# Optimization experiments

Hardware: AMD Instinct MI355X
Metric: run time of the kernel (lower is better)

## Reference

```python
import jax, jax.numpy as jnp
import numpy as np

N_NODES = 100000
N_EDGES = 3200000
D_FEAT = 256
N_CLASS = 40


def setup_inputs() -> dict:
    key = jax.random.key(0)
    ks = jax.random.split(key, 12)
    x = jax.random.normal(ks[0], (N_NODES, D_FEAT), dtype=jnp.float32)
    edge_src = jax.random.randint(ks[1], (N_EDGES,), 0, N_NODES, dtype=jnp.int32)
    edge_dst = jax.random.randint(ks[2], (N_EDGES,), 0, N_NODES, dtype=jnp.int32)
    edge_weight = jax.random.uniform(ks[3], (N_EDGES,), dtype=jnp.float32)
    s = 1.0 / np.sqrt(D_FEAT)
    W1 = jax.random.normal(ks[4], (D_FEAT, D_FEAT), dtype=jnp.float32) * s
    b1 = jax.random.normal(ks[5], (D_FEAT,), dtype=jnp.float32) * s
    W2 = jax.random.normal(ks[6], (D_FEAT, D_FEAT), dtype=jnp.float32) * s
    b2 = jax.random.normal(ks[7], (D_FEAT,), dtype=jnp.float32) * s
    W3 = jax.random.normal(ks[8], (D_FEAT, D_FEAT), dtype=jnp.float32) * s
    b3 = jax.random.normal(ks[9], (D_FEAT,), dtype=jnp.float32) * s
    Wd = jax.random.normal(ks[10], (D_FEAT, N_CLASS), dtype=jnp.float32) * s
    bd = jax.random.normal(ks[11], (N_CLASS,), dtype=jnp.float32) * s
    return {"x": x, "edge_src": edge_src, "edge_dst": edge_dst,
            "edge_weight": edge_weight, "W1": W1, "b1": b1, "W2": W2,
            "b2": b2, "W3": W3, "b3": b3, "Wd": Wd, "bd": bd}


def reference(x, edge_src, edge_dst, edge_weight, W1, b1, W2, b2, W3, b3, Wd, bd):
    n = x.shape[0]

    def spmm(h):  # sparse adj @ h  via gather + segment-sum on dst
        return jax.ops.segment_sum(edge_weight[:, None] * h[edge_src], edge_dst,
                                   num_segments=n)

    # GraphConvolution: adj @ (x @ W) + b, then ReLU (dropout is eval-mode identity)
    h = jax.nn.relu(spmm(x @ W1) + b1)
    h = jax.nn.relu(spmm(h @ W2) + b2)
    h = jax.nn.relu(spmm(h @ W3) + b3)
    return h @ Wd + bd
```

## Files before the change

### kernel.cpp

```cpp
#include <hip/hip_runtime.h>

#define D 256
#define NCLS 40
#define CAP 96
#define KB 391
#define CAPB 9216

typedef __attribute__((ext_vector_type(8))) short bf16x8;
typedef __attribute__((ext_vector_type(4))) float f32x4;

__device__ __forceinline__ unsigned short f2b(float f) {
    unsigned u = __float_as_uint(f);
    u += 0x7fffu + ((u >> 16) & 1u);
    return (unsigned short)(u >> 16);
}
__device__ __forceinline__ float b2f(unsigned short s) {
    return __uint_as_float(((unsigned)s) << 16);
}

__global__ __launch_bounds__(256) void bin_pass1(const int* __restrict__ src,
                                                 const int* __restrict__ dst,
                                                 const float* __restrict__ w, int ne,
                                                 int* __restrict__ bcur,
                                                 int2* __restrict__ binned) {
    __shared__ int cnt[KB], base[KB], cnt2[KB];
    const int tid = threadIdx.x;
    const int e0 = blockIdx.x * 8192;
    for (int i = tid; i < KB; i += 256) { cnt[i] = 0; cnt2[i] = 0; }
    __syncthreads();
    for (int i = tid; i < 8192; i += 256) {
        int e = e0 + i;
        if (e < ne) atomicAdd(&cnt[dst[e] >> 8], 1);
    }
    __syncthreads();
    for (int i = tid; i < KB; i += 256) {
        int c = cnt[i];
        base[i] = c ? atomicAdd(&bcur[i], c) : 0;
    }
    __syncthreads();
    for (int i = tid; i < 8192; i += 256) {
        int e = e0 + i;
        if (e < ne) {
            int d = dst[e];
            int b = d >> 8;
            int slot = base[b] + atomicAdd(&cnt2[b], 1);
            if (slot < CAPB)
                binned[(size_t)b * CAPB + slot] =
                    make_int2((src[e] & 0x1ffff) | ((d & 255) << 17), __float_as_int(w[e]));
        }
    }
}

__global__ __launch_bounds__(256) void bin_pass2(const int2* __restrict__ binned,
                                                 const int* __restrict__ bcur,
                                                 int* __restrict__ cursor,
                                                 int2* __restrict__ pairs, int M) {
    __shared__ int cur[256];
    const int b = blockIdx.x;
    const int tid = threadIdx.x;
    cur[tid] = 0;
    __syncthreads();
    int n = bcur[b]; if (n > CAPB) n = CAPB;
    const int2* rec = binned + (size_t)b * CAPB;
    const int dbase = b << 8;
    for (int i = tid; i < n; i += 256) {
        int2 rc = rec[i];
        int dl = (rc.x >> 17) & 255;
        int s = rc.x & 0x1ffff;
        int r = atomicAdd(&cur[dl], 1);
        if (r < CAP) pairs[(size_t)(dbase + dl) * CAP + r] = make_int2(s, rc.y);
    }
    __syncthreads();
    int d = dbase + tid;
    if (d < M) cursor[d] = min(cur[tid], CAP);
}

__global__ __launch_bounds__(256) void prep_weights3x(const float* __restrict__ W1,
                                                      const float* __restrict__ W2,
                                                      const float* __restrict__ W3,
                                                      short* __restrict__ B1,
                                                      short* __restrict__ B2,
                                                      short* __restrict__ B3) {
    int gi = blockIdx.x * 256 + threadIdx.x;
    int which = gi >> 16;
    int i = gi & 65535;
    const float* W = (which == 0) ? W1 : (which == 1) ? W2 : W3;
    short* Bp      = (which == 0) ? B1 : (which == 1) ? B2 : B3;
    int e = i & 7, lane = (i >> 3) & 63, t = (i >> 9) & 15, ks = (i >> 13) & 7;
    int n = t * 16 + (lane & 15);
    int k = ks * 32 + ((lane >> 4) & 3) * 8 + e;
    Bp[i] = (short)f2b(W[k * D + n]);
}

__global__ __launch_bounds__(256) void prep_wd(const float* __restrict__ Wd,
                                               short* __restrict__ Wdp) {
    int i = blockIdx.x * 256 + threadIdx.x;
    int e = i & 7, lane = (i >> 3) & 63;
    int q = i >> 9;
    int t = q % 3, hl = (q / 3) & 1, ks = q / 6;
    int n = t * 16 + (lane & 15);
    int k = ks * 32 + ((lane >> 4) & 3) * 8 + e;
    float v = (n < NCLS) ? Wd[k * NCLS + n] : 0.f;
    unsigned short hi = f2b(v);
    Wdp[i] = hl ? (short)f2b(v - b2f(hi)) : (short)hi;
}

template<int AFP32>
__global__ __launch_bounds__(256) void gemm_mfma6(const float* __restrict__ A32,
                                                  const short* __restrict__ A16,
                                                  const short* __restrict__ Bpack,
                                                  short* __restrict__ Cout, int M,
                                                  float* __restrict__ sAbs) {
    __shared__ short Bs[2][16384];
    const int tid = threadIdx.x;
    const int lane = tid & 63;
    const int r = lane & 15, kg = lane >> 4;
    const int wv = tid >> 6;
    const int row_base = blockIdx.x * 128 + wv * 32;
    int ar0 = row_base + r;      if (ar0 >= M) ar0 = M - 1;
    int ar1 = row_base + 16 + r; if (ar1 >= M) ar1 = M - 1;

    f32x4 acc0[16], acc1[16];
#pragma unroll
    for (int t = 0; t < 16; t++) {
        acc0[t] = (f32x4){0.f, 0.f, 0.f, 0.f};
        acc1[t] = (f32x4){0.f, 0.f, 0.f, 0.f};
    }

    bf16x8 af0[8], af1[8];
    if (!AFP32) {
#pragma unroll
        for (int ks = 0; ks < 8; ks++) {
            af0[ks] = *(const bf16x8*)(A16 + (size_t)ar0 * D + ks * 32 + kg * 8);
            af1[ks] = *(const bf16x8*)(A16 + (size_t)ar1 * D + ks * 32 + kg * 8);
        }
    }

    auto stage = [&](int step, int buf) {
        const short* src = Bpack + step * 16384 + tid * 8;
        short* dst = &Bs[buf][tid * 8];
#pragma unroll
        for (int j = 0; j < 8; j++) {
            __builtin_amdgcn_global_load_lds(
                (const __attribute__((address_space(1))) unsigned*)(src + j * 2048),
                (__attribute__((address_space(3))) unsigned*)(dst + j * 2048),
                16, 0, 0);
        }
    };

    stage(0, 0);
#pragma unroll
    for (int step = 0; step < 4; step++) {
        __syncthreads();
        if (step < 3) stage(step + 1, (step + 1) & 1);
#pragma unroll
        for (int kh = 0; kh < 2; kh++) {
            const int ks = step * 2 + kh;
            bf16x8 a0k, a1k;
            if (AFP32) {
                const float* p0 = A32 + (size_t)ar0 * D + ks * 32 + kg * 8;
                const float* p1 = A32 + (size_t)ar1 * D + ks * 32 + kg * 8;
                float4 x0 = *(const float4*)p0, x1 = *(const float4*)(p0 + 4);
                float4 y0 = *(const float4*)p1, y1 = *(const float4*)(p1 + 4);
                a0k[0] = (short)f2b(x0.x); a0k[1] = (short)f2b(x0.y);
                a0k[2] = (short)f2b(x0.z); a0k[3] = (short)f2b(x0.w);
                a0k[4] = (short)f2b(x1.x); a0k[5] = (short)f2b(x1.y);
                a0k[6] = (short)f2b(x1.z); a0k[7] = (short)f2b(x1.w);
                a1k[0] = (short)f2b(y0.x); a1k[1] = (short)f2b(y0.y);
                a1k[2] = (short)f2b(y0.z); a1k[3] = (short)f2b(y0.w);
                a1k[4] = (short)f2b(y1.x); a1k[5] = (short)f2b(y1.y);
                a1k[6] = (short)f2b(y1.z); a1k[7] = (short)f2b(y1.w);
            } else {
                a0k = af0[ks];
                a1k = af1[ks];
            }
#pragma unroll
            for (int t = 0; t < 16; t++) {
                bf16x8 h8 = *(const bf16x8*)&Bs[step & 1][kh * 8192 + t * 512 + lane * 8];
                acc0[t] = __builtin_amdgcn_mfma_f32_16x16x32_bf16(a0k, h8, acc0[t], 0, 0, 0);
                acc1[t] = __builtin_amdgcn_mfma_f32_16x16x32_bf16(a1k, h8, acc1[t], 0, 0, 0);
            }
        }
    }

    float m = 0.f;
#pragma unroll
    for (int t = 0; t < 16; t++) {
#pragma unroll
        for (int rg = 0; rg < 4; rg++) {
            m = fmaxf(m, fabsf(acc0[t][rg]));
            m = fmaxf(m, fabsf(acc1[t][rg]));
        }
    }
#pragma unroll
    for (int off = 32; off >= 1; off >>= 1) m = fmaxf(m, __shfl_xor(m, off));
    if (lane == 0) atomicMax((unsigned int*)sAbs, __float_as_uint(m));

#pragma unroll
    for (int t = 0; t < 16; t++) {
#pragma unroll
        for (int rg = 0; rg < 4; rg++) {
            int o0 = row_base + kg * 4 + rg;
            int o1 = o0 + 16;
            if (o0 < M) Cout[(size_t)o0 * D + t * 16 + r] = (short)f2b(acc0[t][rg]);
            if (o1 < M) Cout[(size_t)o1 * D + t * 16 + r] = (short)f2b(acc1[t][rg]);
        }
    }
}

__global__ __launch_bounds__(256) void quant8(const short* __restrict__ hA,
                                              const float* __restrict__ sAbs,
                                              char* __restrict__ h8, int n) {
    int i = (blockIdx.x * 256 + threadIdx.x) * 16;
    if (i >= n) return;
    const float qs = 127.0f / sAbs[0];
    bf16x8 a = *(const bf16x8*)(hA + i);
    bf16x8 b = *(const bf16x8*)(hA + i + 8);
    unsigned pk[4];
#pragma unroll
    for (int d = 0; d < 4; d++) {
        unsigned v = 0;
#pragma unroll
        for (int j = 0; j < 4; j++) {
            int idx = d * 4 + j;
            float f = b2f((unsigned short)(idx < 8 ? a[idx] : b[idx - 8]));
            int q = __float2int_rn(f * qs);
            q = max(-127, min(127, q));
            v |= ((unsigned)(q & 0xff)) << (j * 8);
        }
        pk[d] = v;
    }
    *(uint4*)(h8 + i) = make_uint4(pk[0], pk[1], pk[2], pk[3]);
}

__global__ __launch_bounds__(256) void spmm8q(const char* __restrict__ h8,
                                              const float* __restrict__ sAbs,
                                              const int* __restrict__ cursor,
                                              const int2* __restrict__ pairs,
                                              const float* __restrict__ bias,
                                              short* __restrict__ out, int M) {
    const int node = blockIdx.x * 16 + (threadIdx.x >> 4);
    if (node >= M) return;
    const int t = threadIdx.x & 15;
    int cnt = cursor[node]; if (cnt > CAP) cnt = CAP;
    const int2* pp = pairs + (size_t)node * CAP;
    const size_t doff = (size_t)t * 16;
    const float sc = sAbs[0] * (1.0f / 127.0f);

    float a[16];
#pragma unroll
    for (int j = 0; j < 16; j++) a[j] = 0.f;

#define ACCD(U, B)                                                         \
    {                                                                      \
        unsigned u = (U);                                                  \
        a[(B) + 0] = fmaf(ws, (float)(int)(char)(u), a[(B) + 0]);          \
        a[(B) + 1] = fmaf(ws, (float)(int)(char)(u >> 8), a[(B) + 1]);     \
        a[(B) + 2] = fmaf(ws, (float)(int)(char)(u >> 16), a[(B) + 2]);    \
        a[(B) + 3] = fmaf(ws, (float)((int)u >> 24), a[(B) + 3]);          \
    }
#define ACCQ(V, WB)                                                        \
    {                                                                      \
        float ws = __int_as_float(WB) * sc;                                \
        ACCD((V).x, 0) ACCD((V).y, 4) ACCD((V).z, 8) ACCD((V).w, 12)       \
    }

    int e = 0;
    for (; e + 8 <= cnt; e += 8) {
        int4 q0 = *(const int4*)(pp + e);
        int4 q1 = *(const int4*)(pp + e + 2);
        int4 q2 = *(const int4*)(pp + e + 4);
        int4 q3 = *(const int4*)(pp + e + 6);
        uint4 v0 = *(const uint4*)(h8 + ((size_t)q0.x << 8) + doff);
        uint4 v1 = *(const uint4*)(h8 + ((size_t)q0.z << 8) + doff);
        uint4 v2 = *(const uint4*)(h8 + ((size_t)q1.x << 8) + doff);
        uint4 v3 = *(const uint4*)(h8 + ((size_t)q1.z << 8) + doff);
        uint4 v4 = *(const uint4*)(h8 + ((size_t)q2.x << 8) + doff);
        uint4 v5 = *(const uint4*)(h8 + ((size_t)q2.z << 8) + doff);
        uint4 v6 = *(const uint4*)(h8 + ((size_t)q3.x << 8) + doff);
        uint4 v7 = *(const uint4*)(h8 + ((size_t)q3.z << 8) + doff);
        ACCQ(v0, q0.y) ACCQ(v1, q0.w) ACCQ(v2, q1.y) ACCQ(v3, q1.w)
        ACCQ(v4, q2.y) ACCQ(v5, q2.w) ACCQ(v6, q3.y) ACCQ(v7, q3.w)
    }
    for (; e < cnt; e++) {
        int2 p = pp[e];
        uint4 v = *(const uint4*)(h8 + ((size_t)p.x << 8) + doff);
        ACCQ(v, p.y)
    }
#undef ACCQ
#undef ACCD

    unsigned o[8];
#pragma unroll
    for (int j = 0; j < 8; j++) {
        float2 b = *(const float2*)(bias + t * 16 + j * 2);
        float r0 = fmaxf(a[j * 2] + b.x, 0.f);
        float r1 = fmaxf(a[j * 2 + 1] + b.y, 0.f);
        o[j] = (unsigned)f2b(r0) | ((unsigned)f2b(r1) << 16);
    }
    uint4* dst = (uint4*)(out + ((size_t)node << 8) + doff);
    dst[0] = make_uint4(o[0], o[1], o[2], o[3]);
    dst[1] = make_uint4(o[4], o[5], o[6], o[7]);
}

__global__ __launch_bounds__(256) void dense_mfma(const short* __restrict__ h,
                                                  const short* __restrict__ Wdp,
                                                  const float* __restrict__ bd,
                                                  float* __restrict__ out, int M) {
    __shared__ short Ws[24576];
    const int tid = threadIdx.x;
    const int lane = tid & 63;
    const int r = lane & 15, kg = lane >> 4;
    const int row_base = blockIdx.x * 64 + (tid >> 6) * 16;
    int arow = row_base + r; if (arow >= M) arow = M - 1;

#pragma unroll
    for (int j = 0; j < 12; j++) {
        __builtin_amdgcn_global_load_lds(
            (const __attribute__((address_space(1))) unsigned*)(Wdp + j * 2048 + tid * 8),
            (__attribute__((address_space(3))) unsigned*)(&Ws[j * 2048 + tid * 8]),
            16, 0, 0);
    }

    f32x4 acc[3];
#pragma unroll
    for (int t = 0; t < 3; t++) acc[t] = (f32x4){0.f, 0.f, 0.f, 0.f};

    bf16x8 af[8];
#pragma unroll
    for (int ks = 0; ks < 8; ks++)
        af[ks] = *(const bf16x8*)(h + (size_t)arow * D + ks * 32 + kg * 8);

    __syncthreads();

#pragma unroll
    for (int ks = 0; ks < 8; ks++) {
#pragma unroll
        for (int t = 0; t < 3; t++) {
            bf16x8 h8 = *(const bf16x8*)&Ws[(ks * 6 + t) * 512 + lane * 8];
            bf16x8 l8 = *(const bf16x8*)&Ws[(ks * 6 + 3 + t) * 512 + lane * 8];
            acc[t] = __builtin_amdgcn_mfma_f32_16x16x32_bf16(af[ks], h8, acc[t], 0, 0, 0);
            acc[t] = __builtin_amdgcn_mfma_f32_16x16x32_bf16(af[ks], l8, acc[t], 0, 0, 0);
        }
    }

#pragma unroll
    for (int t = 0; t < 3; t++) {
#pragma unroll
        for (int rg = 0; rg < 4; rg++) {
            int orow = row_base + kg * 4 + rg;
            int col = t * 16 + r;
            if (orow < M && col < NCLS)
                out[(size_t)orow * NCLS + col] = acc[t][rg] + bd[col];
        }
    }
}


extern "C" void kernel_launch(void* const* d_in, const int* in_sizes, int n_in,
                              void* d_out, int out_size, void* d_ws, size_t ws_size,
                              hipStream_t stream) {
    const float* x    = (const float*)d_in[0];
    const int*   esrc = (const int*)d_in[1];
    const int*   edst = (const int*)d_in[2];
    const float* ew   = (const float*)d_in[3];
    const float* W1   = (const float*)d_in[4];
    const float* b1   = (const float*)d_in[5];
    const float* W2   = (const float*)d_in[6];
    const float* b2   = (const float*)d_in[7];
    const float* W3   = (const float*)d_in[8];
    const float* b3   = (const float*)d_in[9];
    const float* Wd   = (const float*)d_in[10];
    const float* bd   = (const float*)d_in[11];
    float* out = (float*)d_out;

    const int M  = in_sizes[0] / D;
    const int NE = in_sizes[1];

    char* p = (char*)d_ws;
    auto alloc = [&](size_t bytes) -> char* {
        char* r = p;
        p += (bytes + 255) & ~(size_t)255;
        return r;
    };
    short* hA     = (short*)alloc((size_t)M * D * sizeof(short));
    short* hB     = (short*)alloc((size_t)M * D * sizeof(short));
    char*  hA8    = (char*)alloc((size_t)M * D);
    int2*  pairs  = (int2*)alloc((size_t)M * CAP * sizeof(int2));
    int2*  binned = (int2*)alloc((size_t)KB * CAPB * sizeof(int2));
    int*   cursor = (int*)alloc((size_t)M * sizeof(int));
    int*   bcur   = (int*)alloc(KB * sizeof(int));
    float* sAbs   = (float*)alloc(256);
    short* B1p = (short*)alloc(D * D * sizeof(short));
    short* B2p = (short*)alloc(D * D * sizeof(short));
    short* B3p = (short*)alloc(D * D * sizeof(short));
    short* Wdp = (short*)alloc(24576 * sizeof(short));

    hipMemsetAsync(bcur, 0, KB * sizeof(int), stream);
    hipMemsetAsync(sAbs, 0, 256, stream);

    bin_pass1<<<(NE + 8191) / 8192, 256, 0, stream>>>(esrc, edst, ew, NE, bcur, binned);
    bin_pass2<<<KB, 256, 0, stream>>>(binned, bcur, cursor, pairs, M);

    prep_weights3x<<<768, 256, 0, stream>>>(W1, W2, W3, B1p, B2p, B3p);
    prep_wd<<<96, 256, 0, stream>>>(Wd, Wdp);

    const int gg = (M + 127) / 128;
    const int gq = (M * D / 16 + 255) / 256;
    const int gs = (M + 15) / 16;

    gemm_mfma6<1><<<gg, 256, 0, stream>>>(x, nullptr, B1p, hA, M, sAbs + 0);
    quant8<<<gq, 256, 0, stream>>>(hA, sAbs + 0, hA8, M * D);
    spmm8q<<<gs, 256, 0, stream>>>(hA8, sAbs + 0, cursor, pairs, b1, hB, M);

    gemm_mfma6<0><<<gg, 256, 0, stream>>>(nullptr, hB, B2p, hA, M, sAbs + 1);
    quant8<<<gq, 256, 0, stream>>>(hA, sAbs + 1, hA8, M * D);
    spmm8q<<<gs, 256, 0, stream>>>(hA8, sAbs + 1, cursor, pairs, b2, hB, M);

    gemm_mfma6<0><<<gg, 256, 0, stream>>>(nullptr, hB, B3p, hA, M, sAbs + 2);
    quant8<<<gq, 256, 0, stream>>>(hA, sAbs + 2, hA8, M * D);
    spmm8q<<<gs, 256, 0, stream>>>(hA8, sAbs + 2, cursor, pairs, b3, hB, M);

    dense_mfma<<<(M + 63) / 64, 256, 0, stream>>>(hB, Wdp, bd, out, M);
}
```

Measured before the change: 716.7 us.

## Fuse int8 quantization into GEMM epilogue with per-block scales

```diff
diff --git a/kernel.cpp b/kernel.cpp
--- a/kernel.cpp
+++ b/kernel.cpp
@@ -106,12 +106,13 @@
 }
 
 template<int AFP32>
-__global__ __launch_bounds__(256) void gemm_mfma6(const float* __restrict__ A32,
+__global__ __launch_bounds__(256) void gemm_mfma7(const float* __restrict__ A32,
                                                   const short* __restrict__ A16,
                                                   const short* __restrict__ Bpack,
-                                                  short* __restrict__ Cout, int M,
-                                                  float* __restrict__ sAbs) {
+                                                  char* __restrict__ C8, int M,
+                                                  float* __restrict__ scales) {
     __shared__ short Bs[2][16384];
+    __shared__ float red[4];
     const int tid = threadIdx.x;
     const int lane = tid & 63;
     const int r = lane & 15, kg = lane >> 4;
@@ -140,7 +141,14 @@
         const short* src = Bpack + step * 16384 + tid * 8;
         short* dst = &Bs[buf][tid * 8];
 #pragma unroll
-        for (int j = 0; j < 8; j++) {
+        for (int j = 0; j < 4; j++) {
+            __builtin_amdgcn_global_load_lds(
+                (const __attribute__((address_space(1))) unsigned*)(src + j * 2048),
+                (__attribute__((address_space(3))) unsigned*)(dst + j * 2048),
+                16, 0, 0);
+        }
+#pragma unroll
+        for (int j = 4; j < 8; j++) {
             __builtin_amdgcn_global_load_lds(
                 (const __attribute__((address_space(1))) unsigned*)(src + j * 2048),
                 (__attribute__((address_space(3))) unsigned*)(dst + j * 2048),
@@ -194,58 +202,51 @@
     }
 #pragma unroll
     for (int off = 32; off >= 1; off >>= 1) m = fmaxf(m, __shfl_xor(m, off));
-    if (lane == 0) atomicMax((unsigned int*)sAbs, __float_as_uint(m));
-
+    if (lane == 0) red[wv] = m;
+    __syncthreads();
+    float bm = fmaxf(fmaxf(red[0], red[1]), fmaxf(red[2], red[3]));
+    float qs = (bm > 0.f) ? 127.0f / bm : 0.f;
+    if (tid == 0) scales[blockIdx.x] = (bm > 0.f) ? bm * (1.0f / 127.0f) : 1.0f;
+
+    char* Q = (char*)&Bs[0][0];
 #pragma unroll
     for (int t = 0; t < 16; t++) {
 #pragma unroll
         for (int rg = 0; rg < 4; rg++) {
-            int o0 = row_base + kg * 4 + rg;
-            int o1 = o0 + 16;
-            if (o0 < M) Cout[(size_t)o0 * D + t * 16 + r] = (short)f2b(acc0[t][rg]);
-            if (o1 < M) Cout[(size_t)o1 * D + t * 16 + r] = (short)f2b(acc1[t][rg]);
-        }
-    }
-}
-
-__global__ __launch_bounds__(256) void quant8(const short* __restrict__ hA,
-                                              const float* __restrict__ sAbs,
-                                              char* __restrict__ h8, int n) {
-    int i = (blockIdx.x * 256 + threadIdx.x) * 16;
-    if (i >= n) return;
-    const float qs = 127.0f / sAbs[0];
-    bf16x8 a = *(const bf16x8*)(hA + i);
-    bf16x8 b = *(const bf16x8*)(hA + i + 8);
-    unsigned pk[4];
-#pragma unroll
-    for (int d = 0; d < 4; d++) {
-        unsigned v = 0;
-#pragma unroll
-        for (int j = 0; j < 4; j++) {
-            int idx = d * 4 + j;
-            float f = b2f((unsigned short)(idx < 8 ? a[idx] : b[idx - 8]));
-            int q = __float2int_rn(f * qs);
-            q = max(-127, min(127, q));
-            v |= ((unsigned)(q & 0xff)) << (j * 8);
-        }
-        pk[d] = v;
-    }
-    *(uint4*)(h8 + i) = make_uint4(pk[0], pk[1], pk[2], pk[3]);
-}
-
-__global__ __launch_bounds__(256) void spmm8q(const char* __restrict__ h8,
-                                              const float* __restrict__ sAbs,
-                                              const int* __restrict__ cursor,
-                                              const int2* __restrict__ pairs,
-                                              const float* __restrict__ bias,
-                                              short* __restrict__ out, int M) {
+            int rl = wv * 32 + kg * 4 + rg;
+            int q0 = __float2int_rn(acc0[t][rg] * qs);
+            q0 = max(-127, min(127, q0));
+            Q[rl * 272 + t * 16 + r] = (char)q0;
+            int q1 = __float2int_rn(acc1[t][rg] * qs);
+            q1 = max(-127, min(127, q1));
+            Q[(rl + 16) * 272 + t * 16 + r] = (char)q1;
+        }
+    }
+    __syncthreads();
+
+    const int nl = tid >> 1;
+    const int c0 = (tid & 1) * 128;
+    const int grow = blockIdx.x * 128 + nl;
+    if (grow < M) {
+        uint4* dst = (uint4*)(C8 + (size_t)grow * 256 + c0);
+        const char* qs_ = &Q[nl * 272 + c0];
+#pragma unroll
+        for (int j = 0; j < 8; j++) dst[j] = *(const uint4*)(qs_ + j * 16);
+    }
+}
+
+__global__ __launch_bounds__(256) void spmm8q2(const char* __restrict__ h8,
+                                               const float* __restrict__ scales,
+                                               const int* __restrict__ cursor,
+                                               const int2* __restrict__ pairs,
+                                               const float* __restrict__ bias,
+                                               short* __restrict__ out, int M) {
     const int node = blockIdx.x * 16 + (threadIdx.x >> 4);
     if (node >= M) return;
     const int t = threadIdx.x & 15;
     int cnt = cursor[node]; if (cnt > CAP) cnt = CAP;
     const int2* pp = pairs + (size_t)node * CAP;
     const size_t doff = (size_t)t * 16;
-    const float sc = sAbs[0] * (1.0f / 127.0f);
 
     float a[16];
 #pragma unroll
@@ -259,9 +260,9 @@
         a[(B) + 2] = fmaf(ws, (float)(int)(char)(u >> 16), a[(B) + 2]);    \
         a[(B) + 3] = fmaf(ws, (float)((int)u >> 24), a[(B) + 3]);          \
     }
-#define ACCQ(V, WB)                                                        \
+#define ACCQ(V, WB, SRC)                                                   \
     {                                                                      \
-        float ws = __int_as_float(WB) * sc;                                \
+        float ws = __int_as_float(WB) * scales[(SRC) >> 7];                \
         ACCD((V).x, 0) ACCD((V).y, 4) ACCD((V).z, 8) ACCD((V).w, 12)       \
     }
 
@@ -279,13 +280,15 @@
         uint4 v5 = *(const uint4*)(h8 + ((size_t)q2.z << 8) + doff);
         uint4 v6 = *(const uint4*)(h8 + ((size_t)q3.x << 8) + doff);
         uint4 v7 = *(const uint4*)(h8 + ((size_t)q3.z << 8) + doff);
-        ACCQ(v0, q0.y) ACCQ(v1, q0.w) ACCQ(v2, q1.y) ACCQ(v3, q1.w)
-        ACCQ(v4, q2.y) ACCQ(v5, q2.w) ACCQ(v6, q3.y) ACCQ(v7, q3.w)
+        ACCQ(v0, q0.y, q0.x) ACCQ(v1, q0.w, q0.z)
+        ACCQ(v2, q1.y, q1.x) ACCQ(v3, q1.w, q1.z)
+        ACCQ(v4, q2.y, q2.x) ACCQ(v5, q2.w, q2.z)
+        ACCQ(v6, q3.y, q3.x) ACCQ(v7, q3.w, q3.z)
     }
     for (; e < cnt; e++) {
         int2 p = pp[e];
         uint4 v = *(const uint4*)(h8 + ((size_t)p.x << 8) + doff);
-        ACCQ(v, p.y)
+        ACCQ(v, p.y, p.x)
     }
 #undef ACCQ
 #undef ACCD
@@ -383,21 +386,19 @@
         p += (bytes + 255) & ~(size_t)255;
         return r;
     };
-    short* hA     = (short*)alloc((size_t)M * D * sizeof(short));
     short* hB     = (short*)alloc((size_t)M * D * sizeof(short));
     char*  hA8    = (char*)alloc((size_t)M * D);
     int2*  pairs  = (int2*)alloc((size_t)M * CAP * sizeof(int2));
     int2*  binned = (int2*)alloc((size_t)KB * CAPB * sizeof(int2));
     int*   cursor = (int*)alloc((size_t)M * sizeof(int));
     int*   bcur   = (int*)alloc(KB * sizeof(int));
-    float* sAbs   = (float*)alloc(256);
+    float* scales = (float*)alloc(1024 * sizeof(float));
     short* B1p = (short*)alloc(D * D * sizeof(short));
     short* B2p = (short*)alloc(D * D * sizeof(short));
     short* B3p = (short*)alloc(D * D * sizeof(short));
     short* Wdp = (short*)alloc(24576 * sizeof(short));
 
     hipMemsetAsync(bcur, 0, KB * sizeof(int), stream);
-    hipMemsetAsync(sAbs, 0, 256, stream);
 
     bin_pass1<<<(NE + 8191) / 8192, 256, 0, stream>>>(esrc, edst, ew, NE, bcur, binned);
     bin_pass2<<<KB, 256, 0, stream>>>(binned, bcur, cursor, pairs, M);
@@ -406,20 +407,16 @@
     prep_wd<<<96, 256, 0, stream>>>(Wd, Wdp);
 
     const int gg = (M + 127) / 128;
-    const int gq = (M * D / 16 + 255) / 256;
     const int gs = (M + 15) / 16;
 
-    gemm_mfma6<1><<<gg, 256, 0, stream>>>(x, nullptr, B1p, hA, M, sAbs + 0);
-    quant8<<<gq, 256, 0, stream>>>(hA, sAbs + 0, hA8, M * D);
-    spmm8q<<<gs, 256, 0, stream>>>(hA8, sAbs + 0, cursor, pairs, b1, hB, M);
-
-    gemm_mfma6<0><<<gg, 256, 0, stream>>>(nullptr, hB, B2p, hA, M, sAbs + 1);
-    quant8<<<gq, 256, 0, stream>>>(hA, sAbs + 1, hA8, M * D);
-    spmm8q<<<gs, 256, 0, stream>>>(hA8, sAbs + 1, cursor, pairs, b2, hB, M);
-
-    gemm_mfma6<0><<<gg, 256, 0, stream>>>(nullptr, hB, B3p, hA, M, sAbs + 2);
-    quant8<<<gq, 256, 0, stream>>>(hA, sAbs + 2, hA8, M * D);
-    spmm8q<<<gs, 256, 0, stream>>>(hA8, sAbs + 2, cursor, pairs, b3, hB, M);
+    gemm_mfma7<1><<<gg, 256, 0, stream>>>(x, nullptr, B1p, hA8, M, scales);
+    spmm8q2<<<gs, 256, 0, stream>>>(hA8, scales, cursor, pairs, b1, hB, M);
+
+    gemm_mfma7<0><<<gg, 256, 0, stream>>>(nullptr, hB, B2p, hA8, M, scales);
+    spmm8q2<<<gs, 256, 0, stream>>>(hA8, scales, cursor, pairs, b2, hB, M);
+
+    gemm_mfma7<0><<<gg, 256, 0, stream>>>(nullptr, hB, B3p, hA8, M, scales);
+    spmm8q2<<<gs, 256, 0, stream>>>(hA8, scales, cursor, pairs, b3, hB, M);
 
     dense_mfma<<<(M + 63) / 64, 256, 0, stream>>>(hB, Wdp, bd, out, M);
 }
```

Result: faster. 683.2 us (-4.7%).
